# Optimization experiments

Hardware: AMD Instinct MI355X
Metric: run time of the kernel (lower is better)

The kernel has to match this reference:

```python
import jax, jax.numpy as jnp
import numpy as np

B, L, S = 1, 2048, 2048
D_MODEL, H = 1024, 16
DK = D_MODEL // H  # d_keys = d_values = 64


def sparsemax(z):
    # sparsemax along last axis: proj of z onto the simplex
    K = z.shape[-1]
    z_sorted = jnp.flip(jnp.sort(z, axis=-1), axis=-1)
    cs = jnp.cumsum(z_sorted, axis=-1)
    r = jnp.arange(1, K + 1, dtype=z.dtype)
    support = 1.0 + r * z_sorted > cs
    k = jnp.sum(support, axis=-1, keepdims=True)
    tau = (jnp.take_along_axis(cs, k.astype(jnp.int32) - 1, axis=-1) - 1.0) / k.astype(z.dtype)
    return jnp.maximum(z - tau, 0.0)


def setup_inputs() -> dict:
    key = jax.random.key(0)
    ks = jax.random.split(key, 12)
    sc = 1.0 / np.sqrt(D_MODEL)
    return {
        "queries": jax.random.normal(ks[0], (B, L, D_MODEL), jnp.float32),
        "keys": jax.random.normal(ks[1], (B, S, D_MODEL), jnp.float32),
        "values": jax.random.normal(ks[2], (B, S, D_MODEL), jnp.float32),
        "Wq": jax.random.normal(ks[3], (D_MODEL, H * DK), jnp.float32) * sc,
        "bq": jnp.zeros((H * DK,), jnp.float32),
        "Wk": jax.random.normal(ks[4], (D_MODEL, H * DK), jnp.float32) * sc,
        "bk": jnp.zeros((H * DK,), jnp.float32),
        "Wv": jax.random.normal(ks[5], (H * DK, H * DK), jnp.float32) * sc,
        "bv": jnp.zeros((H * DK,), jnp.float32),
        "Wo": jax.random.normal(ks[6], (H * DK, D_MODEL), jnp.float32) * sc,
        "bo": jnp.zeros((D_MODEL,), jnp.float32),
    }


def reference(queries, keys, values, Wq, bq, Wk, bk, Wv, bv, Wo, bo):
    # projections (note: input `values` is unused, matching the torch source)
    q = (queries @ Wq + bq).reshape(B, L, H, DK)
    k_flat = keys @ Wk + bk                      # [B,S,H*DK]
    k = k_flat.reshape(B, S, H, DK)
    v = (k_flat @ Wv + bv).reshape(B, S, H, DK)  # value_projection(key_projection(keys))
    scale = 1.0 / np.sqrt(DK)
    scores = jnp.einsum('blhe,bshe->bhls', q, k) * scale  # [B,H,L,S]
    A = sparsemax(scores)
    out = jnp.einsum('bhls,bshd->blhd', A, v)             # [B,L,H,DK]
    # mix=True: transpose(2,1) -> [B,H,L,D] then view(B,L,-1)
    out = jnp.swapaxes(out, 1, 2).reshape(B, L, H * DK)
    return out @ Wo + bo
```

## Files before the change

### kernel.cpp

```cpp
#include <hip/hip_runtime.h>
#include <hip/hip_bf16.h>


typedef __attribute__((ext_vector_type(8))) short short8;
typedef __attribute__((ext_vector_type(4))) float floatx4;

#define SRC_BF16 0
#define SRC_F32  1
#define SRC_RT   2
#define NSEG 3
#define OVF 64
#define CAPT (64 * NSEG + OVF)

__device__ __forceinline__ short f2bf(float f) {
    __hip_bfloat16 h = __float2bfloat16(f);
    return *reinterpret_cast<const short*>(&h);
}
__device__ __forceinline__ unsigned short f2bfu(float f) {
    __hip_bfloat16 h = __float2bfloat16(f);
    return *reinterpret_cast<const unsigned short*>(&h);
}
__device__ __forceinline__ float bf2f(unsigned short u) {
    return __uint_as_float(((unsigned)u) << 16);
}
__device__ __forceinline__ unsigned fmap(float f) {
    unsigned u = __float_as_uint(f);
    return (u & 0x80000000u) ? ~u : (u | 0x80000000u);
}
__device__ __forceinline__ float funmap(unsigned u) {
    return (u & 0x80000000u) ? __uint_as_float(u ^ 0x80000000u) : __uint_as_float(~u);
}

__global__ void detect_k(const short* __restrict__ q, int n, int* __restrict__ flag)
{
    const int tid = threadIdx.x;
    int bad = 0;
    for (int i = tid; i < n; i += 64) {
        float f = bf2f((unsigned short)q[i]);
        if (!(fabsf(f) < 1e10f)) bad = 1;
    }
    unsigned long long m = __ballot(bad != 0);
    if (tid == 0) *flag = (m != 0ULL) ? 1 : 0;
}

__global__ __launch_bounds__(256)
void convert2_k(const void* __restrict__ s0, const void* __restrict__ s1,
                short* __restrict__ d0, short* __restrict__ d1,
                const int* __restrict__ dflag)
{
    const void* s = blockIdx.z ? s1 : s0;
    short* d = blockIdx.z ? d1 : d0;
    const size_t i = ((size_t)blockIdx.x * 256 + threadIdx.x) * 8;
    short8 o;
    if (*dflag) {
        const float4 f0 = ((const float4*)((const float*)s + i))[0];
        const float4 f1 = ((const float4*)((const float*)s + i))[1];
        o[0] = f2bf(f0.x); o[1] = f2bf(f0.y); o[2] = f2bf(f0.z); o[3] = f2bf(f0.w);
        o[4] = f2bf(f1.x); o[5] = f2bf(f1.y); o[6] = f2bf(f1.z); o[7] = f2bf(f1.w);
    } else {
        o = *(const short8*)((const short*)s + i);
    }
    *(short8*)(d + i) = o;
}

struct TP4 {
    const void* s[4];
    short* d[4];
};
__global__ __launch_bounds__(256)
void transpose4_k(TP4 p, int R, int C, const int* __restrict__ dflag)
{
    __shared__ short T[64][72];
    const int tid = threadIdx.x;
    const int bC = blockIdx.x, bR = blockIdx.y;
    const void* src = p.s[blockIdx.z];
    short* dst = p.d[blockIdx.z];
    const bool f32 = (*dflag != 0);

    const int colg = (tid & 7) * 8;
    #pragma unroll
    for (int h = 0; h < 2; ++h) {
        const int row = (tid >> 3) + 32 * h;
        const size_t idx = (size_t)(bR * 64 + row) * (size_t)C + (size_t)(bC * 64 + colg);
        short e[8];
        if (f32) {
            const float4 f0 = ((const float4*)((const float*)src + idx))[0];
            const float4 f1 = ((const float4*)((const float*)src + idx))[1];
            e[0] = f2bf(f0.x); e[1] = f2bf(f0.y); e[2] = f2bf(f0.z); e[3] = f2bf(f0.w);
            e[4] = f2bf(f1.x); e[5] = f2bf(f1.y); e[6] = f2bf(f1.z); e[7] = f2bf(f1.w);
        } else {
            short8 s = *(const short8*)((const short*)src + idx);
            #pragma unroll
            for (int j = 0; j < 8; ++j) e[j] = s[j];
        }
        #pragma unroll
        for (int j = 0; j < 8; ++j) T[colg + j][row] = e[j];
    }
    __syncthreads();
    #pragma unroll
    for (int h = 0; h < 2; ++h) {
        const int orow = (tid >> 3) + 32 * h;
        const int ocolg = (tid & 7) * 8;
        const size_t idx = (size_t)(bC * 64 + orow) * (size_t)R + (size_t)(bR * 64 + ocolg);
        *(short8*)(dst + idx) = *(const short8*)&T[orow][ocolg];
    }
}

struct GJ { const short* A; const short* B; const void* bias; void* C; float os; };

template<int OSRC>
__global__ __launch_bounds__(256)
void gemm64_bt_k(GJ j0, GJ j1, const int* __restrict__ dflag)
{
    __shared__ __align__(16) short As[64][40];
    __shared__ __align__(16) short Bs[64][40];

    const GJ j = blockIdx.z ? j1 : j0;
    const int rtf = *dflag;

    const int tid  = threadIdx.x;
    const int bN   = blockIdx.x, bM = blockIdx.y;
    const int lane = tid & 63, wave = tid >> 6;
    const int wm   = (wave >> 1) * 32;
    const int wn   = (wave & 1) * 32;
    const int quad = lane >> 4, r16 = lane & 15;

    floatx4 acc[2][2];
    #pragma unroll
    for (int i = 0; i < 2; ++i)
        #pragma unroll
        for (int jj = 0; jj < 2; ++jj)
            acc[i][jj] = (floatx4){0.f, 0.f, 0.f, 0.f};

    const int ar = tid >> 2, ac = (tid & 3) * 8;

    for (int k0 = 0; k0 < 1024; k0 += 32) {
        *(short8*)&As[ar][ac] =
            *(const short8*)(j.A + (size_t)(bM * 64 + ar) * 1024 + (size_t)(k0 + ac));
        *(short8*)&Bs[ar][ac] =
            *(const short8*)(j.B + (size_t)(bN * 64 + ar) * 1024 + (size_t)(k0 + ac));
        __syncthreads();

        short8 a0 = *(const short8*)&As[wm + r16][quad * 8];
        short8 a1 = *(const short8*)&As[wm + 16 + r16][quad * 8];
        short8 b0 = *(const short8*)&Bs[wn + r16][quad * 8];
        short8 b1 = *(const short8*)&Bs[wn + 16 + r16][quad * 8];

        acc[0][0] = __builtin_amdgcn_mfma_f32_16x16x32_bf16(a0, b0, acc[0][0], 0, 0, 0);
        acc[0][1] = __builtin_amdgcn_mfma_f32_16x16x32_bf16(a0, b1, acc[0][1], 0, 0, 0);
        acc[1][0] = __builtin_amdgcn_mfma_f32_16x16x32_bf16(a1, b0, acc[1][0], 0, 0, 0);
        acc[1][1] = __builtin_amdgcn_mfma_f32_16x16x32_bf16(a1, b1, acc[1][1], 0, 0, 0);
        __syncthreads();
    }

    const bool of32 = (OSRC == SRC_F32) || (OSRC == SRC_RT && rtf);
    #pragma unroll
    for (int jj = 0; jj < 2; ++jj) {
        const int gc = bN * 64 + wn + jj * 16 + r16;
        const float bb = rtf ? ((const float*)j.bias)[gc]
                             : bf2f(((const unsigned short*)j.bias)[gc]);
        #pragma unroll
        for (int i = 0; i < 2; ++i) {
            #pragma unroll
            for (int rg = 0; rg < 4; ++rg) {
                const int gr = bM * 64 + wm + i * 16 + quad * 4 + rg;
                const float v = (acc[i][jj][rg] + bb) * j.os;
                if (of32)
                    ((float*)j.C)[(size_t)gr * 1024 + gc] = v;
                else
                    ((__hip_bfloat16*)j.C)[(size_t)gr * 1024 + gc] = __float2bfloat16(v);
            }
        }
    }
}

__global__ __launch_bounds__(256, 8)
void attn_fused_k(const short* __restrict__ Qb, const short* __restrict__ Kb,
                  const short* __restrict__ Vb, short* __restrict__ Ob)
{
    __shared__ unsigned cpk[16][CAPT];
    __shared__ unsigned rmax[16];
    __shared__ int cnt[16];

    const int tid  = threadIdx.x;
    const int lane = tid & 63, wave = tid >> 6;
    const int quad = lane >> 4, r16 = lane & 15;

    const int bid  = blockIdx.x;
    const int slot = bid >> 3;
    const int h    = (slot & 1) * 8 + (bid & 7);
    const int row0 = (slot >> 1) * 16;

    if (tid < 16) { rmax[tid] = fmap(-3.0e38f); cnt[tid] = 0; }
    __syncthreads();

    const short* qp = Qb + (size_t)(row0 + r16) * 1024 + h * 64 + quad * 8;
    const short8 qa0 = *(const short8*)qp;
    const short8 qa1 = *(const short8*)(qp + 32);

    const int myrow = quad * 4;
    const int wid   = wave * 16 + r16;
    const short* kp0 = Kb + (size_t)(wave * 16 + r16) * 1024 + h * 64 + quad * 8;

    float rm1[4], rm2[4];
    int mycnt[4];
    #pragma unroll
    for (int rg = 0; rg < 4; ++rg) { rm1[rg] = -3.0e38f; rm2[rg] = -3.0e38f; mycnt[rg] = 0; }

    for (int s0 = 0; s0 < 2048; s0 += 256) {
        floatx4 acc[4];
        #pragma unroll
        for (int t = 0; t < 4; ++t) {
            const short* kp = kp0 + (size_t)(s0 + t * 64) * 1024;
            const short8 b0 = *(const short8*)kp;
            const short8 b1 = *(const short8*)(kp + 32);
            floatx4 a = (floatx4){0.f, 0.f, 0.f, 0.f};
            a = __builtin_amdgcn_mfma_f32_16x16x32_bf16(qa0, b0, a, 0, 0, 0);
            a = __builtin_amdgcn_mfma_f32_16x16x32_bf16(qa1, b1, a, 0, 0, 0);
            acc[t] = a;
        }

        #pragma unroll
        for (int rg = 0; rg < 4; ++rg) {
            float m1ab = fmaxf(acc[0][rg], acc[1][rg]);
            float m2ab = fminf(acc[0][rg], acc[1][rg]);
            float m1cd = fmaxf(acc[2][rg], acc[3][rg]);
            float m2cd = fminf(acc[2][rg], acc[3][rg]);
            float m1 = fmaxf(m1ab, m1cd);
            float m2 = fmaxf(fminf(m1ab, m1cd), (m1ab >= m1cd) ? m2ab : m2cd);
            #pragma unroll
            for (int off = 1; off < 16; off <<= 1) {
                const float o1 = __shfl_xor(m1, off, 64);
                const float o2 = __shfl_xor(m2, off, 64);
                const float n2 = fmaxf(fminf(m1, o1), (m1 >= o1) ? m2 : o2);
                m1 = fmaxf(m1, o1);
                m2 = n2;
            }
            const float n1 = fmaxf(rm1[rg], m1);
            rm2[rg] = fmaxf(fminf(rm1[rg], m1), (rm1[rg] >= m1) ? rm2[rg] : m2);
            rm1[rg] = n1;
            if (r16 == 0) atomicMax(&rmax[myrow + rg], fmap(m1));
        }

        #pragma unroll
        for (int rg = 0; rg < 4; ++rg) {
            const int row = myrow + rg;
            const float g1 = fmaxf(funmap(rmax[row]), rm1[rg]);
            const float thr = fmaxf(g1 - 1.0f, 0.5f * (g1 + rm2[rg]) - 0.5f);
            #pragma unroll
            for (int t = 0; t < 4; ++t) {
                const float val = acc[t][rg];
                if (val >= thr) {
                    const unsigned pk = ((unsigned)f2bfu(val) << 16)
                                      | (unsigned)(s0 + wave * 16 + t * 64 + r16);
                    const int c = mycnt[rg];
                    if (c < NSEG) {
                        cpk[row][wid * NSEG + c] = pk;
                    } else {
                        const int p = atomicAdd(&cnt[row], 1);
                        if (p < OVF) cpk[row][64 * NSEG + p] = pk;
                    }
                    mycnt[rg] = c + 1;
                }
            }
        }
    }

    #pragma unroll
    for (int rg = 0; rg < 4; ++rg) {
        const int row = myrow + rg;
        for (int k = mycnt[rg]; k < NSEG; ++k)
            cpk[row][wid * NSEG + k] = 0xFF800000u;
    }
    __syncthreads();

    const unsigned long long pre = (1ULL << lane) - 1ULL;
    for (int rr = 0; rr < 4; ++rr) {
        const int r = wave * 4 + rr;
        const int novf = min(cnt[r], OVF);

        float v[4];
        unsigned short ii[4];
        #pragma unroll
        for (int i = 0; i < 3; ++i) {
            const unsigned u = cpk[r][lane + i * 64];
            v[i] = bf2f((unsigned short)(u >> 16));
            ii[i] = (unsigned short)(u & 0xFFFFu);
        }
        if (lane < novf) {
            const unsigned u = cpk[r][64 * NSEG + lane];
            v[3] = bf2f((unsigned short)(u >> 16));
            ii[3] = (unsigned short)(u & 0xFFFFu);
        } else { v[3] = -3.0e38f; ii[3] = 0; }

        float tau = funmap(rmax[r]) - 1.0f, prevc = -1.0f;
        for (int it = 0; it < 24; ++it) {
            float s = 0.f, c = 0.f;
            #pragma unroll
            for (int i = 0; i < 4; ++i)
                if (v[i] > tau) { s += v[i]; c += 1.f; }
            #pragma unroll
            for (int off = 1; off < 64; off <<= 1) {
                s += __shfl_xor(s, off, 64);
                c += __shfl_xor(c, off, 64);
            }
            if (c == prevc) break;
            prevc = c;
            tau = (s - 1.0f) / c;
        }

        int base = 0;
        #pragma unroll
        for (int i = 0; i < 4; ++i) {
            const float p = v[i] - tau;
            const unsigned long long m = __ballot(p > 0.f);
            const int w = base + __popcll(m & pre);
            if (p > 0.f) cpk[r][w] = ((unsigned)f2bfu(p) << 16) | (unsigned)ii[i];
            base += __popcll(m);
        }
        const int msup = base;

        const unsigned short* vb = (const unsigned short*)Vb + (size_t)h * 64 + lane;
        float o0 = 0.f, o1 = 0.f, o2 = 0.f, o3 = 0.f;
        int jj = 0;
        for (; jj + 4 <= msup; jj += 4) {
            const unsigned u0 = cpk[r][jj],     u1 = cpk[r][jj + 1];
            const unsigned u2 = cpk[r][jj + 2], u3 = cpk[r][jj + 3];
            o0 += bf2f((unsigned short)(u0 >> 16)) * bf2f(vb[(size_t)(u0 & 0xFFFFu) * 1024]);
            o1 += bf2f((unsigned short)(u1 >> 16)) * bf2f(vb[(size_t)(u1 & 0xFFFFu) * 1024]);
            o2 += bf2f((unsigned short)(u2 >> 16)) * bf2f(vb[(size_t)(u2 & 0xFFFFu) * 1024]);
            o3 += bf2f((unsigned short)(u3 >> 16)) * bf2f(vb[(size_t)(u3 & 0xFFFFu) * 1024]);
        }
        for (; jj < msup; ++jj) {
            const unsigned u0 = cpk[r][jj];
            o0 += bf2f((unsigned short)(u0 >> 16)) * bf2f(vb[(size_t)(u0 & 0xFFFFu) * 1024]);
        }
        Ob[((size_t)h * 2048 + row0 + r) * 64 + lane] = f2bf(o0 + o1 + o2 + o3);
    }
}

extern "C" void kernel_launch(void* const* d_in, const int* in_sizes, int n_in,
                              void* d_out, int out_size, void* d_ws, size_t ws_size,
                              hipStream_t stream)
{
    (void)in_sizes; (void)n_in; (void)out_size; (void)ws_size;

    const void* queries = d_in[0];
    const void* keys    = d_in[1];
    const void* Wq = d_in[3];
    const void* bq = d_in[4];
    const void* Wk = d_in[5];
    const void* bk = d_in[6];
    const void* Wv = d_in[7];
    const void* bv = d_in[8];
    const void* Wo = d_in[9];
    const void* bo = d_in[10];

    const int L = 2048, DM = 1024;
    const size_t LD = (size_t)L * DM;

    int*   flag = (int*)d_ws;
    short* Qc  = (short*)((char*)d_ws + 256);
    short* Kc  = Qc + LD;
    short* WqT = Kc + LD;
    short* WkT = WqT + (size_t)DM * DM;
    short* WvT = WkT + (size_t)DM * DM;
    short* WoT = WvT + (size_t)DM * DM;
    short* Qb  = WoT + (size_t)DM * DM;
    short* Kb  = Qb + LD;
    short* Vb  = Kb + LD;
    short* Ob  = Vb + LD;

    dim3 blk(256);

    detect_k<<<dim3(1), dim3(64), 0, stream>>>((const short*)queries, 4096, flag);

    convert2_k<<<dim3((unsigned)(LD / 2048), 1, 2), blk, 0, stream>>>(
        queries, keys, Qc, Kc, flag);

    {
        TP4 p;
        p.s[0] = Wq; p.s[1] = Wk; p.s[2] = Wv; p.s[3] = Wo;
        p.d[0] = WqT; p.d[1] = WkT; p.d[2] = WvT; p.d[3] = WoT;
        transpose4_k<<<dim3(DM / 64, DM / 64, 4), blk, 0, stream>>>(p, DM, DM, flag);
    }

    {
        GJ jq{(const short*)Qc, WqT, bq, Qb, 0.125f};
        GJ jk{(const short*)Kc, WkT, bk, Kb, 1.0f};
        gemm64_bt_k<SRC_BF16><<<dim3(DM / 64, L / 64, 2), blk, 0, stream>>>(jq, jk, flag);
    }
    {
        GJ jv{(const short*)Kb, WvT, bv, Vb, 1.0f};
        gemm64_bt_k<SRC_BF16><<<dim3(DM / 64, L / 64, 1), blk, 0, stream>>>(jv, jv, flag);
    }

    attn_fused_k<<<dim3((L / 16) * 16), blk, 0, stream>>>(Qb, Kb, Vb, Ob);

    {
        GJ jo{(const short*)Ob, WoT, bo, d_out, 1.0f};
        gemm64_bt_k<SRC_RT><<<dim3(DM / 64, L / 64, 1), blk, 0, stream>>>(jo, jo, flag);
    }
}
```

Before: 279.8 us.

## Double-buffer GEMM tiles via direct global-to-LDS loads and unroll sparse AV gather

The projection GEMM now uses global_load_lds to copy K=64 tiles straight into XOR-swizzled LDS double buffers, so the next tile's load overlaps the current tile's MFMAs and the number of barriers per K-step is halved. The sparse A·V accumulation loop is unrolled to 8 independent accumulators to keep more gathered V loads in flight. This raises LDS use, relies on the swizzle matching the direct-load lane layout, and slightly changes the floating-point summation order.

```diff
diff --git a/kernel.cpp b/kernel.cpp
--- a/kernel.cpp
+++ b/kernel.cpp
@@ -11,6 +11,10 @@
 #define NSEG 3
 #define OVF 64
 #define CAPT (64 * NSEG + OVF)
+
+typedef __attribute__((address_space(1))) const void GAS;
+typedef __attribute__((address_space(3))) void LAS;
+#define GLOAD16(g, l) __builtin_amdgcn_global_load_lds((GAS*)(g), (LAS*)(l), 16, 0, 0)
 
 __device__ __forceinline__ short f2bf(float f) {
     __hip_bfloat16 h = __float2bfloat16(f);
@@ -112,8 +116,8 @@
 __global__ __launch_bounds__(256)
 void gemm64_bt_k(GJ j0, GJ j1, const int* __restrict__ dflag)
 {
-    __shared__ __align__(16) short As[64][40];
-    __shared__ __align__(16) short Bs[64][40];
+    __shared__ __align__(16) short As[2][64][64];
+    __shared__ __align__(16) short Bs[2][64][64];
 
     const GJ j = blockIdx.z ? j1 : j0;
     const int rtf = *dflag;
@@ -132,26 +136,45 @@
         for (int jj = 0; jj < 2; ++jj)
             acc[i][jj] = (floatx4){0.f, 0.f, 0.f, 0.f};
 
-    const int ar = tid >> 2, ac = (tid & 3) * 8;
-
-    for (int k0 = 0; k0 < 1024; k0 += 32) {
-        *(short8*)&As[ar][ac] =
-            *(const short8*)(j.A + (size_t)(bM * 64 + ar) * 1024 + (size_t)(k0 + ac));
-        *(short8*)&Bs[ar][ac] =
-            *(const short8*)(j.B + (size_t)(bN * 64 + ar) * 1024 + (size_t)(k0 + ac));
+    const int srow = wave * 8 + (lane >> 3);
+    const int scg  = (lane & 7) ^ ((lane >> 3) & 7);
+    const short* gA = j.A + (size_t)(bM * 64 + srow) * 1024 + scg * 8;
+    const short* gB = j.B + (size_t)(bN * 64 + srow) * 1024 + scg * 8;
+
+#define STAGE(buf, k0)                                                          \
+    {                                                                           \
+        _Pragma("unroll")                                                       \
+        for (int jj = 0; jj < 2; ++jj) {                                        \
+            GLOAD16(gA + (size_t)jj * 32 * 1024 + (k0),                         \
+                    &As[buf][wave * 8 + jj * 32][0]);                           \
+            GLOAD16(gB + (size_t)jj * 32 * 1024 + (k0),                         \
+                    &Bs[buf][wave * 8 + jj * 32][0]);                           \
+        }                                                                       \
+    }
+
+    STAGE(0, 0);
+    __syncthreads();
+
+    const int sr = r16 & 7;
+    int buf = 0;
+    for (int t = 0; t < 16; ++t) {
+        if (t < 15) STAGE(buf ^ 1, (t + 1) * 64);
+        #pragma unroll
+        for (int kk = 0; kk < 2; ++kk) {
+            const int pc = ((kk * 4 + quad) ^ sr) * 8;
+            const short8 a0 = *(const short8*)&As[buf][wm + r16][pc];
+            const short8 a1 = *(const short8*)&As[buf][wm + 16 + r16][pc];
+            const short8 b0 = *(const short8*)&Bs[buf][wn + r16][pc];
+            const short8 b1 = *(const short8*)&Bs[buf][wn + 16 + r16][pc];
+            acc[0][0] = __builtin_amdgcn_mfma_f32_16x16x32_bf16(a0, b0, acc[0][0], 0, 0, 0);
+            acc[0][1] = __builtin_amdgcn_mfma_f32_16x16x32_bf16(a0, b1, acc[0][1], 0, 0, 0);
+            acc[1][0] = __builtin_amdgcn_mfma_f32_16x16x32_bf16(a1, b0, acc[1][0], 0, 0, 0);
+            acc[1][1] = __builtin_amdgcn_mfma_f32_16x16x32_bf16(a1, b1, acc[1][1], 0, 0, 0);
+        }
         __syncthreads();
-
-        short8 a0 = *(const short8*)&As[wm + r16][quad * 8];
-        short8 a1 = *(const short8*)&As[wm + 16 + r16][quad * 8];
-        short8 b0 = *(const short8*)&Bs[wn + r16][quad * 8];
-        short8 b1 = *(const short8*)&Bs[wn + 16 + r16][quad * 8];
-
-        acc[0][0] = __builtin_amdgcn_mfma_f32_16x16x32_bf16(a0, b0, acc[0][0], 0, 0, 0);
-        acc[0][1] = __builtin_amdgcn_mfma_f32_16x16x32_bf16(a0, b1, acc[0][1], 0, 0, 0);
-        acc[1][0] = __builtin_amdgcn_mfma_f32_16x16x32_bf16(a1, b0, acc[1][0], 0, 0, 0);
-        acc[1][1] = __builtin_amdgcn_mfma_f32_16x16x32_bf16(a1, b1, acc[1][1], 0, 0, 0);
-        __syncthreads();
-    }
+        buf ^= 1;
+    }
+#undef STAGE
 
     const bool of32 = (OSRC == SRC_F32) || (OSRC == SRC_RT && rtf);
     #pragma unroll
@@ -322,20 +345,28 @@
 
         const unsigned short* vb = (const unsigned short*)Vb + (size_t)h * 64 + lane;
         float o0 = 0.f, o1 = 0.f, o2 = 0.f, o3 = 0.f;
+        float o4 = 0.f, o5 = 0.f, o6 = 0.f, o7 = 0.f;
         int jj = 0;
-        for (; jj + 4 <= msup; jj += 4) {
+        for (; jj + 8 <= msup; jj += 8) {
             const unsigned u0 = cpk[r][jj],     u1 = cpk[r][jj + 1];
             const unsigned u2 = cpk[r][jj + 2], u3 = cpk[r][jj + 3];
+            const unsigned u4 = cpk[r][jj + 4], u5 = cpk[r][jj + 5];
+            const unsigned u6 = cpk[r][jj + 6], u7 = cpk[r][jj + 7];
             o0 += bf2f((unsigned short)(u0 >> 16)) * bf2f(vb[(size_t)(u0 & 0xFFFFu) * 1024]);
             o1 += bf2f((unsigned short)(u1 >> 16)) * bf2f(vb[(size_t)(u1 & 0xFFFFu) * 1024]);
             o2 += bf2f((unsigned short)(u2 >> 16)) * bf2f(vb[(size_t)(u2 & 0xFFFFu) * 1024]);
             o3 += bf2f((unsigned short)(u3 >> 16)) * bf2f(vb[(size_t)(u3 & 0xFFFFu) * 1024]);
+            o4 += bf2f((unsigned short)(u4 >> 16)) * bf2f(vb[(size_t)(u4 & 0xFFFFu) * 1024]);
+            o5 += bf2f((unsigned short)(u5 >> 16)) * bf2f(vb[(size_t)(u5 & 0xFFFFu) * 1024]);
+            o6 += bf2f((unsigned short)(u6 >> 16)) * bf2f(vb[(size_t)(u6 & 0xFFFFu) * 1024]);
+            o7 += bf2f((unsigned short)(u7 >> 16)) * bf2f(vb[(size_t)(u7 & 0xFFFFu) * 1024]);
         }
         for (; jj < msup; ++jj) {
             const unsigned u0 = cpk[r][jj];
             o0 += bf2f((unsigned short)(u0 >> 16)) * bf2f(vb[(size_t)(u0 & 0xFFFFu) * 1024]);
         }
-        Ob[((size_t)h * 2048 + row0 + r) * 64 + lane] = f2bf(o0 + o1 + o2 + o3);
+        const float out = ((o0 + o1) + (o2 + o3)) + ((o4 + o5) + (o6 + o7));
+        Ob[((size_t)h * 2048 + row0 + r) * 64 + lane] = f2bf(out);
     }
 }
 
```

New measurement: 269.0 us. 1.04x faster.
